# Performance work log

Hardware: AMD Instinct MI355X
Metric: run time of the kernel (lower is better)

The kernel has to match this reference:

```python
import jax, jax.numpy as jnp
import numpy as np

B, S, D, H = 2, 2048, 1024, 16
HD = D // H  # head_dim = 64


def setup_inputs() -> dict:
    key = jax.random.key(0)
    ks = jax.random.split(key, 6)
    scale = 0.02
    return {
        "x": jax.random.normal(ks[0], (B, S, D), dtype=jnp.float32),
        "wq": jax.random.normal(ks[1], (D, D), dtype=jnp.float32) * scale,  # torch Linear weight [out,in]
        "wk": jax.random.normal(ks[2], (D, D), dtype=jnp.float32) * scale,
        "wv": jax.random.normal(ks[3], (D, D), dtype=jnp.float32) * scale,
        "wo": jax.random.normal(ks[4], (D, D), dtype=jnp.float32) * scale,
        "bo": jnp.zeros((D,), dtype=jnp.float32),
    }


def reference(x, wq, wk, wv, wo, bo):
    b, t, d = x.shape
    # projections (torch nn.Linear: x @ W.T), split into heads -> [b, h, t, hd]
    def split_heads(y):
        return y.reshape(b, t, H, HD).transpose(0, 2, 1, 3)

    q = split_heads(x @ wq.T)
    k = split_heads(x @ wk.T)
    v = split_heads(x @ wv.T)

    scores = jnp.einsum("bhqd,bhkd->bhqk", q, k)  # [b,h,t,t]
    causal = jnp.triu(jnp.ones((t, t), dtype=bool), k=1)
    scores = jnp.where(causal, -jnp.inf, scores)
    attn = jax.nn.softmax(scores / jnp.sqrt(jnp.asarray(HD, scores.dtype)), axis=-1)
    # dropout p=0.0 -> identity (eval-mode reference)
    ctx = jnp.einsum("bhqk,bhkd->bhqd", attn, v)
    ctx = ctx.transpose(0, 2, 1, 3).reshape(b, t, d)
    return ctx @ wo.T + bo
```

## Files before the change

### kernel.cpp

```cpp
#include <hip/hip_runtime.h>
#include <hip/hip_bf16.h>
#include <stdint.h>
#include <math.h>

#define NH   16
#define HDIM 64
#define SEQ  2048
#define DM   1024
#define NB   2
#define MTOK (NB * SEQ)

typedef __bf16 bf16x8 __attribute__((ext_vector_type(8)));
typedef float  f32x4  __attribute__((ext_vector_type(4)));

__device__ __forceinline__ unsigned short f2bf(float f) {
  union { float f; unsigned int u; } c; c.f = f;
  unsigned int u = c.u;
  return (unsigned short)((u + 0x7FFFu + ((u >> 16) & 1u)) >> 16);
}
__device__ __forceinline__ unsigned int pk2bf(float a, float b) {
  __hip_bfloat162 h = __float22bfloat162_rn(float2{a, b});
  return *reinterpret_cast<unsigned int*>(&h);
}

__device__ __forceinline__ void async_copy16(const void* g, void* l) {
  __builtin_amdgcn_global_load_lds((__attribute__((address_space(1))) void*)g,
                                   (__attribute__((address_space(3))) void*)l,
                                   16, 0, 0);
}

__global__ void cast_all(const float* __restrict__ x,  const float* __restrict__ wq,
                         const float* __restrict__ wk, const float* __restrict__ wv,
                         const float* __restrict__ wo,
                         unsigned short* __restrict__ xb,
                         unsigned short* __restrict__ wqkvb,
                         unsigned short* __restrict__ wob) {
  const int seg = blockIdx.y;
  const float* src;
  unsigned short* dst;
  int n4;
  if (seg == 0)      { src = x;  dst = xb;                  n4 = MTOK * DM / 4; }
  else if (seg == 1) { src = wq; dst = wqkvb;               n4 = DM * DM / 4; }
  else if (seg == 2) { src = wk; dst = wqkvb + DM * DM;     n4 = DM * DM / 4; }
  else if (seg == 3) { src = wv; dst = wqkvb + 2 * DM * DM; n4 = DM * DM / 4; }
  else               { src = wo; dst = wob;                 n4 = DM * DM / 4; }
  const int i = blockIdx.x * blockDim.x + threadIdx.x;
  if (i >= n4) return;
  float4 v = reinterpret_cast<const float4*>(src)[i];
  uint2 o;
  o.x = pk2bf(v.x, v.y); o.y = pk2bf(v.z, v.w);
  reinterpret_cast<uint2*>(dst)[i] = o;
}

#define QSCALE 0.1803368801111244f
template <int MODE>
__global__ __launch_bounds__(256, 2) void gemm_bt(
    const unsigned short* __restrict__ A,
    const unsigned short* __restrict__ B,
    unsigned short* __restrict__ qo, unsigned short* __restrict__ ko,
    unsigned short* __restrict__ vo,
    float* __restrict__ co, const float* __restrict__ bias,
    int M, int N, int K) {
  __shared__ __align__(16) unsigned short As[128 * 32];
  __shared__ __align__(16) unsigned short Bs[128 * 32];

  const int tid  = threadIdx.x;
  const int lane = tid & 63;
  const int wave = tid >> 6;
  const int l15  = lane & 15;
  const int quad = lane >> 4;
  const int wm   = (wave >> 1) * 64;
  const int wn   = (wave & 1) * 64;
  const int m0   = blockIdx.x * 128;
  const int n0   = blockIdx.y * 128;

  f32x4 acc[4][4];
#pragma unroll
  for (int a = 0; a < 4; ++a)
#pragma unroll
    for (int b = 0; b < 4; ++b) acc[a][b] = f32x4{0.f, 0.f, 0.f, 0.f};

  for (int k0 = 0; k0 < K; k0 += 32) {
    __syncthreads();
#pragma unroll
    for (int s = 0; s < 2; ++s) {
      const int c   = tid + s * 256;
      const int row = c >> 2;
      const int col = (c & 3) * 8;
      unsigned short* lA = As + ((size_t)wave * 64 + s * 256) * 8;
      unsigned short* lB = Bs + ((size_t)wave * 64 + s * 256) * 8;
      async_copy16(A + (size_t)(m0 + row) * K + k0 + col, lA);
      async_copy16(B + (size_t)(n0 + row) * K + k0 + col, lB);
    }
    __syncthreads();

    bf16x8 af[4], bfr[4];
#pragma unroll
    for (int t = 0; t < 4; ++t) {
      af[t]  = *reinterpret_cast<const bf16x8*>(As + (wm + t * 16 + l15) * 32 + quad * 8);
      bfr[t] = *reinterpret_cast<const bf16x8*>(Bs + (wn + t * 16 + l15) * 32 + quad * 8);
    }
#pragma unroll
    for (int ti = 0; ti < 4; ++ti)
#pragma unroll
      for (int tj = 0; tj < 4; ++tj)
        acc[ti][tj] = __builtin_amdgcn_mfma_f32_16x16x32_bf16(af[ti], bfr[tj], acc[ti][tj], 0, 0, 0);
  }

#pragma unroll
  for (int ti = 0; ti < 4; ++ti) {
#pragma unroll
    for (int tj = 0; tj < 4; ++tj) {
      const int mb = m0 + wm + ti * 16 + quad * 4;
      const int n  = n0 + wn + tj * 16 + l15;
      if (MODE == 0) {
        const int which = n >> 10;
        const int n1 = n & 1023;
        const int h = n1 >> 6, d = n1 & 63;
        const int b = mb >> 11, s = mb & 2047;
        if (which == 0) {
          const size_t idx = ((size_t)(b * NH + h) * SEQ + s) * HDIM + d;
#pragma unroll
          for (int r = 0; r < 4; ++r) qo[idx + (size_t)r * HDIM] = f2bf(acc[ti][tj][r] * QSCALE);
        } else if (which == 1) {
          const size_t idx = ((size_t)(b * NH + h) * SEQ + s) * HDIM + d;
#pragma unroll
          for (int r = 0; r < 4; ++r) ko[idx + (size_t)r * HDIM] = f2bf(acc[ti][tj][r]);
        } else {
          const size_t idx = ((size_t)(b * NH + h) * HDIM + d) * SEQ + s;
          uint2 pk;
          pk.x = pk2bf(acc[ti][tj][0], acc[ti][tj][1]);
          pk.y = pk2bf(acc[ti][tj][2], acc[ti][tj][3]);
          *reinterpret_cast<uint2*>(vo + idx) = pk;
        }
      } else {
#pragma unroll
        for (int r = 0; r < 4; ++r)
          co[(size_t)(mb + r) * N + n] = acc[ti][tj][r] + bias[n];
      }
    }
  }
}

#define KST 72
#define PST 72

__global__ __launch_bounds__(256, 5) void flash_attn_mfma(
    const unsigned short* __restrict__ Qb,
    const unsigned short* __restrict__ Kb,
    const unsigned short* __restrict__ Vtg,
    unsigned short* __restrict__ ctx) {
  __shared__ __align__(16) unsigned short Ks[64 * KST];
  __shared__ __align__(16) unsigned short Vt[64 * KST];
  __shared__ __align__(16) unsigned short Pt[4][16 * PST];

  const int tid  = threadIdx.x;
  const int qt   = gridDim.x - 1 - blockIdx.x;
  const int bh   = blockIdx.y;
  const int q0   = qt * 64;
  const int lane = tid & 63;
  const int wave = tid >> 6;
  const int l15  = lane & 15;
  const int quad = lane >> 4;

  const size_t baseQK = (size_t)bh * SEQ * HDIM;
  const size_t baseV  = (size_t)bh * HDIM * SEQ;

  const int srow = tid >> 3;
  const int scol = (tid & 7) * 8;

  bf16x8 qf[2];
  {
    const unsigned short* qp = Qb + baseQK + (size_t)(q0 + wave * 16 + l15) * HDIM + quad * 8;
    qf[0] = *reinterpret_cast<const bf16x8*>(qp);
    qf[1] = *reinterpret_cast<const bf16x8*>(qp + 32);
  }

  float l_acc = 0.f;
  f32x4 o[4];
#pragma unroll
  for (int td = 0; td < 4; ++td) o[td] = f32x4{0.f, 0.f, 0.f, 0.f};

  for (int kt = 0; kt <= qt; ++kt) {
    __syncthreads();
    {
      const uint4 k0v = *reinterpret_cast<const uint4*>(Kb + baseQK + (size_t)(kt * 64 + srow) * HDIM + scol);
      const uint4 k1v = *reinterpret_cast<const uint4*>(Kb + baseQK + (size_t)(kt * 64 + srow + 32) * HDIM + scol);
      const uint4 v0v = *reinterpret_cast<const uint4*>(Vtg + baseV + (size_t)srow * SEQ + kt * 64 + scol);
      const uint4 v1v = *reinterpret_cast<const uint4*>(Vtg + baseV + (size_t)(srow + 32) * SEQ + kt * 64 + scol);
      *reinterpret_cast<uint4*>(&Ks[srow * KST + scol]) = k0v;
      *reinterpret_cast<uint4*>(&Ks[(srow + 32) * KST + scol]) = k1v;
      *reinterpret_cast<uint4*>(&Vt[srow * KST + scol]) = v0v;
      *reinterpret_cast<uint4*>(&Vt[(srow + 32) * KST + scol]) = v1v;
    }
    __syncthreads();

    const int tmax = (kt == qt) ? wave : 3;

    f32x4 st[4];
#pragma unroll
    for (int t = 0; t < 4; ++t) st[t] = f32x4{-INFINITY, -INFINITY, -INFINITY, -INFINITY};
#pragma unroll
    for (int t = 0; t < 4; ++t) {
      if (t <= tmax) {
        f32x4 c = f32x4{0.f, 0.f, 0.f, 0.f};
        const int krow = (t * 16 + l15) * KST;
        const bf16x8 kf0 = *reinterpret_cast<const bf16x8*>(&Ks[krow + quad * 8]);
        const bf16x8 kf1 = *reinterpret_cast<const bf16x8*>(&Ks[krow + 32 + quad * 8]);
        c = __builtin_amdgcn_mfma_f32_16x16x32_bf16(kf0, qf[0], c, 0, 0, 0);
        c = __builtin_amdgcn_mfma_f32_16x16x32_bf16(kf1, qf[1], c, 0, 0, 0);
        if (kt == qt && t == wave) {
#pragma unroll
          for (int r = 0; r < 4; ++r)
            if (quad * 4 + r > l15) c[r] = -INFINITY;
        }
        st[t] = c;
      }
    }

#pragma unroll
    for (int t = 0; t < 4; ++t) {
      const float p0 = exp2f(st[t][0]);
      const float p1 = exp2f(st[t][1]);
      const float p2 = exp2f(st[t][2]);
      const float p3 = exp2f(st[t][3]);
      l_acc += (p0 + p1) + (p2 + p3);
      uint2 pk;
      pk.x = pk2bf(p0, p1);
      pk.y = pk2bf(p2, p3);
      *reinterpret_cast<uint2*>(&Pt[wave][l15 * PST + t * 16 + quad * 4]) = pk;
    }

    const int smax = (kt == qt && wave < 2) ? 0 : 1;
#pragma unroll
    for (int sv = 0; sv < 2; ++sv) {
      if (sv <= smax) {
        const bf16x8 pf = *reinterpret_cast<const bf16x8*>(&Pt[wave][l15 * PST + sv * 32 + quad * 8]);
#pragma unroll
        for (int td = 0; td < 4; ++td) {
          const bf16x8 vf = *reinterpret_cast<const bf16x8*>(&Vt[(td * 16 + l15) * KST + sv * 32 + quad * 8]);
          o[td] = __builtin_amdgcn_mfma_f32_16x16x32_bf16(pf, vf, o[td], 0, 0, 0);
        }
      }
    }
  }

  float l_s = l_acc;
  l_s += __shfl_xor(l_s, 16, 64);
  l_s += __shfl_xor(l_s, 32, 64);
  const float linv = 1.f / l_s;
  const int b = bh >> 4, h = bh & 15;
#pragma unroll
  for (int r = 0; r < 4; ++r) {
    const float lr = __shfl(linv, quad * 4 + r, 64);
    const int sr = q0 + wave * 16 + quad * 4 + r;
    const size_t ob = (size_t)(b * SEQ + sr) * DM + h * HDIM + l15;
#pragma unroll
    for (int td = 0; td < 4; ++td)
      ctx[ob + td * 16] = f2bf(o[td][r] * lr);
  }
}

extern "C" void kernel_launch(void* const* d_in, const int* in_sizes, int n_in,
                              void* d_out, int out_size, void* d_ws, size_t ws_size,
                              hipStream_t stream) {
  const float* x  = (const float*)d_in[0];
  const float* wq = (const float*)d_in[1];
  const float* wk = (const float*)d_in[2];
  const float* wv = (const float*)d_in[3];
  const float* wo = (const float*)d_in[4];
  const float* bo = (const float*)d_in[5];
  float* out = (float*)d_out;

  char* ws = (char*)d_ws;
  unsigned short* xb    = (unsigned short*)(ws);
  unsigned short* wqkvb = (unsigned short*)(ws + (8ull  << 20));
  unsigned short* wob   = (unsigned short*)(ws + (14ull << 20));
  unsigned short* Qb    = (unsigned short*)(ws + (16ull << 20));
  unsigned short* Kb    = (unsigned short*)(ws + (24ull << 20));
  unsigned short* Vtg   = (unsigned short*)(ws + (32ull << 20));
  unsigned short* ctxb  = (unsigned short*)(ws + (40ull << 20));

  dim3 gc(4096, 5);
  cast_all<<<gc, 256, 0, stream>>>(x, wq, wk, wv, wo, xb, wqkvb, wob);

  dim3 g1(MTOK / 128, (3 * DM) / 128);
  gemm_bt<0><<<g1, 256, 0, stream>>>(xb, wqkvb, Qb, Kb, Vtg, nullptr, nullptr,
                                     MTOK, 3 * DM, DM);

  dim3 g2(SEQ / 64, NB * NH);
  flash_attn_mfma<<<g2, 256, 0, stream>>>(Qb, Kb, Vtg, ctxb);

  dim3 g3(MTOK / 128, DM / 128);
  gemm_bt<1><<<g3, 256, 0, stream>>>(ctxb, wob, nullptr, nullptr, nullptr, out, bo,
                                     MTOK, DM, DM);
}
```

Before: 213.2 us.

## Split long causal query tiles across KV chunks and add reduction kernel

The causal flash-attention grid now gives query tiles 12 and above two or three KV chunks of at most 12 tiles each, so no block loops over more than 12 key tiles. This evens out the load between the short early rows and the long late rows. Partial unnormalized outputs (stored as bf16) and row sums go to workspace buffers. A new attn_reduce kernel sums the partials and normalizes them into ctx. The cost is an extra launch, extra global traffic, and bf16 rounding of the partials. The unrescaled sum relies on the kernel not using a per-chunk running max.

```diff
diff --git a/kernel.cpp b/kernel.cpp
--- a/kernel.cpp
+++ b/kernel.cpp
@@ -17,6 +17,10 @@
   union { float f; unsigned int u; } c; c.f = f;
   unsigned int u = c.u;
   return (unsigned short)((u + 0x7FFFu + ((u >> 16) & 1u)) >> 16);
+}
+__device__ __forceinline__ float bf2f(unsigned short s) {
+  union { unsigned int u; float f; } c; c.u = ((unsigned int)s) << 16;
+  return c.f;
 }
 __device__ __forceinline__ unsigned int pk2bf(float a, float b) {
   __hip_bfloat162 h = __float22bfloat162_rn(float2{a, b});
@@ -149,19 +153,30 @@
     const unsigned short* __restrict__ Qb,
     const unsigned short* __restrict__ Kb,
     const unsigned short* __restrict__ Vtg,
-    unsigned short* __restrict__ ctx) {
+    unsigned short* __restrict__ ctx,
+    unsigned short* __restrict__ pO,
+    float* __restrict__ pL) {
   __shared__ __align__(16) unsigned short Ks[64 * KST];
   __shared__ __align__(16) unsigned short Vt[64 * KST];
   __shared__ __align__(16) unsigned short Pt[4][16 * PST];
 
   const int tid  = threadIdx.x;
-  const int qt   = gridDim.x - 1 - blockIdx.x;
   const int bh   = blockIdx.y;
-  const int q0   = qt * 64;
   const int lane = tid & 63;
   const int wave = tid >> 6;
   const int l15  = lane & 15;
   const int quad = lane >> 4;
+
+  int qt, chunk, nch;
+  {
+    const int x = blockIdx.x;
+    if (x < 12)      { qt = x;                 chunk = 0;            nch = 1; }
+    else if (x < 36) { qt = 12 + (x - 12) / 2; chunk = (x - 12) % 2; nch = 2; }
+    else             { qt = 24 + (x - 36) / 3; chunk = (x - 36) % 3; nch = 3; }
+  }
+  const int q0 = qt * 64;
+  const int c0 = chunk * 12;
+  const int c1 = min(qt, c0 + 11);
 
   const size_t baseQK = (size_t)bh * SEQ * HDIM;
   const size_t baseV  = (size_t)bh * HDIM * SEQ;
@@ -181,7 +196,7 @@
 #pragma unroll
   for (int td = 0; td < 4; ++td) o[td] = f32x4{0.f, 0.f, 0.f, 0.f};
 
-  for (int kt = 0; kt <= qt; ++kt) {
+  for (int kt = c0; kt <= c1; ++kt) {
     __syncthreads();
     {
       const uint4 k0v = *reinterpret_cast<const uint4*>(Kb + baseQK + (size_t)(kt * 64 + srow) * HDIM + scol);
@@ -248,17 +263,73 @@
   float l_s = l_acc;
   l_s += __shfl_xor(l_s, 16, 64);
   l_s += __shfl_xor(l_s, 32, 64);
-  const float linv = 1.f / l_s;
+
+  if (nch == 1) {
+    const float linv = 1.f / l_s;
+    const int b = bh >> 4, h = bh & 15;
+#pragma unroll
+    for (int r = 0; r < 4; ++r) {
+      const float lr = __shfl(linv, quad * 4 + r, 64);
+      const int sr = q0 + wave * 16 + quad * 4 + r;
+      const size_t ob = (size_t)(b * SEQ + sr) * DM + h * HDIM + l15;
+#pragma unroll
+      for (int td = 0; td < 4; ++td)
+        ctx[ob + td * 16] = f2bf(o[td][r] * lr);
+    }
+  } else {
+    const int pb = (qt < 24) ? 2 * (qt - 12) : 24 + 3 * (qt - 24);
+    const int pidx = bh * 48 + pb + chunk;
+    if (quad == 0) pL[pidx * 64 + wave * 16 + l15] = l_s;
+    unsigned short* po = pO + (size_t)pidx * 4096;
+#pragma unroll
+    for (int r = 0; r < 4; ++r) {
+      const int ql = wave * 16 + quad * 4 + r;
+#pragma unroll
+      for (int td = 0; td < 4; ++td)
+        po[ql * 64 + td * 16 + l15] = f2bf(o[td][r]);
+    }
+  }
+}
+
+__global__ __launch_bounds__(256, 8) void attn_reduce(
+    const unsigned short* __restrict__ pO, const float* __restrict__ pL,
+    unsigned short* __restrict__ ctx) {
+  const int x = blockIdx.x;
+  int qt, pb, nch;
+  if (x < 12) { qt = 12 + x; pb = 2 * x;            nch = 2; }
+  else        { qt = 24 + (x - 12); pb = 24 + 3 * (x - 12); nch = 3; }
+  const int bh = blockIdx.y;
   const int b = bh >> 4, h = bh & 15;
-#pragma unroll
-  for (int r = 0; r < 4; ++r) {
-    const float lr = __shfl(linv, quad * 4 + r, 64);
-    const int sr = q0 + wave * 16 + quad * 4 + r;
-    const size_t ob = (size_t)(b * SEQ + sr) * DM + h * HDIM + l15;
-#pragma unroll
-    for (int td = 0; td < 4; ++td)
-      ctx[ob + td * 16] = f2bf(o[td][r] * lr);
-  }
+  const int pidx = bh * 48 + pb;
+
+  const int tid = threadIdx.x;
+  const int ql  = tid >> 2;
+  const int d0  = (tid & 3) * 16;
+
+  float acc[16];
+#pragma unroll
+  for (int e = 0; e < 16; ++e) acc[e] = 0.f;
+  float lsum = 0.f;
+
+  for (int c = 0; c < nch; ++c) {
+    lsum += pL[(pidx + c) * 64 + ql];
+    const unsigned short* src = pO + (size_t)(pidx + c) * 4096 + ql * 64 + d0;
+    const uint4 v0 = *reinterpret_cast<const uint4*>(src);
+    const uint4 v1 = *reinterpret_cast<const uint4*>(src + 8);
+    const unsigned short* u = reinterpret_cast<const unsigned short*>(&v0);
+    const unsigned short* w = reinterpret_cast<const unsigned short*>(&v1);
+#pragma unroll
+    for (int e = 0; e < 8; ++e) { acc[e] += bf2f(u[e]); acc[8 + e] += bf2f(w[e]); }
+  }
+
+  const float linv = 1.f / lsum;
+  unsigned int outw[8];
+#pragma unroll
+  for (int e = 0; e < 8; ++e)
+    outw[e] = pk2bf(acc[2 * e] * linv, acc[2 * e + 1] * linv);
+  unsigned short* dst = ctx + (size_t)(b * SEQ + qt * 64 + ql) * DM + h * HDIM + d0;
+  *reinterpret_cast<uint4*>(dst)     = *reinterpret_cast<uint4*>(&outw[0]);
+  *reinterpret_cast<uint4*>(dst + 8) = *reinterpret_cast<uint4*>(&outw[4]);
 }
 
 extern "C" void kernel_launch(void* const* d_in, const int* in_sizes, int n_in,
@@ -280,6 +351,8 @@
   unsigned short* Kb    = (unsigned short*)(ws + (24ull << 20));
   unsigned short* Vtg   = (unsigned short*)(ws + (32ull << 20));
   unsigned short* ctxb  = (unsigned short*)(ws + (40ull << 20));
+  unsigned short* pO    = (unsigned short*)(ws);
+  float*          pL    = (float*)(ws + (12ull << 20));
 
   dim3 gc(4096, 5);
   cast_all<<<gc, 256, 0, stream>>>(x, wq, wk, wv, wo, xb, wqkvb, wob);
@@ -288,8 +361,11 @@
   gemm_bt<0><<<g1, 256, 0, stream>>>(xb, wqkvb, Qb, Kb, Vtg, nullptr, nullptr,
                                      MTOK, 3 * DM, DM);
 
-  dim3 g2(SEQ / 64, NB * NH);
-  flash_attn_mfma<<<g2, 256, 0, stream>>>(Qb, Kb, Vtg, ctxb);
+  dim3 g2(60, NB * NH);
+  flash_attn_mfma<<<g2, 256, 0, stream>>>(Qb, Kb, Vtg, ctxb, pO, pL);
+
+  dim3 gr(20, NB * NH);
+  attn_reduce<<<gr, 256, 0, stream>>>(pO, pL, ctxb);
 
   dim3 g3(MTOK / 128, DM / 128);
   gemm_bt<1><<<g3, 256, 0, stream>>>(ctxb, wob, nullptr, nullptr, nullptr, out, bo,
```

Measured after the change: 201.3 us. 5.6% less time.
